# Performance work log

Measured on AMD Instinct MI355X. Metric: run time of the kernel, lower is better.

Reference implementation:

```python
import jax, jax.numpy as jnp
import numpy as np

PI = 3.14159  # literal used by the original module
N_QUBITS = 3
N_LAYERS = 2


def _apply_ry(state, theta, wire):
    """Apply RY(theta) on `wire`. state: (B, 2, 2, 2). theta: scalar or (B,)."""
    st = jnp.moveaxis(state, wire + 1, -1)
    c = jnp.cos(theta * 0.5)
    s = jnp.sin(theta * 0.5)
    nd = st.ndim - 1  # rank of st[..., 0]
    c = c.reshape(c.shape + (1,) * (nd - c.ndim))
    s = s.reshape(s.shape + (1,) * (nd - s.ndim))
    s0, s1 = st[..., 0], st[..., 1]
    st = jnp.stack([c * s0 - s * s1, s * s0 + c * s1], axis=-1)
    return jnp.moveaxis(st, -1, wire + 1)


def _apply_cnot(state, ctrl, tgt):
    """CNOT with control `ctrl`, target `tgt`: flip target where control=1."""
    st = jnp.moveaxis(state, (ctrl + 1, tgt + 1), (-2, -1))
    st = jnp.stack([st[..., 0, :], st[..., 1, ::-1]], axis=-2)
    return jnp.moveaxis(st, (-2, -1), (ctrl + 1, tgt + 1))


def _circuit(x, weights):
    B = x.shape[0]
    dt = x.dtype
    # |000...0> initial state, batched: (B, 2, 2, 2)
    state = jnp.zeros((B,) + (2,) * N_QUBITS, dt)
    state = state.at[(slice(None),) + (0,) * N_QUBITS].set(1.0)
    # angle encoding: RY(x[:, i] * pi) on wire i
    for i in range(N_QUBITS):
        state = _apply_ry(state, x[:, i] * PI, i)
    # variational layers: RY(weights[l, i]) then CNOT chain
    for l in range(N_LAYERS):
        for i in range(N_QUBITS):
            state = _apply_ry(state, weights[l, i], i)
        for i in range(N_QUBITS - 1):
            state = _apply_cnot(state, i, i + 1)
    # <Z_i> = sum_s |amp_s|^2 * (1 - 2*bit_i(s))  (RY/CNOT keep state real)
    probs = (state * state).reshape(B, 2 ** N_QUBITS)
    idx = jnp.arange(2 ** N_QUBITS)
    bits = (idx[None, :] >> (N_QUBITS - 1 - jnp.arange(N_QUBITS)[:, None])) & 1
    signs = (1.0 - 2.0 * bits).astype(dt)  # (n_qubits, 8)
    return probs @ signs.T  # (B, n_qubits)


def setup_inputs() -> dict:
    key = jax.random.key(0)
    k1, k2 = jax.random.split(key)
    x = jax.random.normal(k1, (2097152, 4), jnp.float32)
    weights = jax.random.normal(k2, (2, 3), jnp.float32) * 0.1
    return {"x": x, "weights": weights}


def reference(x, weights):
    return _circuit(x, weights)
```

## Files before the change

kernel.cpp:

```cpp
#include <hip/hip_runtime.h>


__global__ __launch_bounds__(256) void qfl_kernel(
    const float4* __restrict__ x, const float* __restrict__ w,
    float* __restrict__ out, int n)
{
    __shared__ float swc[6], sws[6];
    __shared__ float sout[768];
    const int tid = threadIdx.x;
    const long long b = (long long)blockIdx.x * 256 + tid;

    if (tid < 6) {
        float t = 0.5f * w[tid];
        sws[tid] = __sinf(t);
        swc[tid] = __cosf(t);
    }
    __syncthreads();

    float4 xv = (b < (long long)n) ? x[b] : make_float4(0.f, 0.f, 0.f, 0.f);

    const float HPI = 0.5f * 3.14159f;
    float a0, a1, b0, b1, c0, c1;
    __sincosf(xv.x * HPI, &a1, &a0);
    __sincosf(xv.y * HPI, &b1, &b0);
    __sincosf(xv.z * HPI, &c1, &c0);

    float st[8];
    st[0] = a0 * b0 * c0; st[1] = a0 * b0 * c1;
    st[2] = a0 * b1 * c0; st[3] = a0 * b1 * c1;
    st[4] = a1 * b0 * c0; st[5] = a1 * b0 * c1;
    st[6] = a1 * b1 * c0; st[7] = a1 * b1 * c1;

    #pragma unroll
    for (int l = 0; l < 2; ++l) {
        {
            float c = swc[l * 3 + 0], s = sws[l * 3 + 0];
            #pragma unroll
            for (int k = 0; k < 4; ++k) {
                float u = st[k], v = st[k + 4];
                st[k] = c * u - s * v; st[k + 4] = s * u + c * v;
            }
        }
        {
            float c = swc[l * 3 + 1], s = sws[l * 3 + 1];
            #pragma unroll
            for (int k = 0; k < 2; ++k) {
                float u = st[k],     v = st[k + 2];
                st[k]     = c * u  - s * v;  st[k + 2] = s * u  + c * v;
                float u2 = st[k + 4], v2 = st[k + 6];
                st[k + 4] = c * u2 - s * v2; st[k + 6] = s * u2 + c * v2;
            }
        }
        {
            float c = swc[l * 3 + 2], s = sws[l * 3 + 2];
            #pragma unroll
            for (int k = 0; k < 8; k += 2) {
                float u = st[k], v = st[k + 1];
                st[k] = c * u - s * v; st[k + 1] = s * u + c * v;
            }
        }
        { float t = st[4]; st[4] = st[6]; st[6] = t;
          t = st[5]; st[5] = st[7]; st[7] = t; }
        { float t = st[2]; st[2] = st[3]; st[3] = t;
          t = st[6]; st[6] = st[7]; st[7] = t; }
    }

    float p[8];
    #pragma unroll
    for (int k = 0; k < 8; ++k) p[k] = st[k] * st[k];
    float o0 = (p[0] + p[1] + p[2] + p[3]) - (p[4] + p[5] + p[6] + p[7]);
    float o1 = (p[0] + p[1] + p[4] + p[5]) - (p[2] + p[3] + p[6] + p[7]);
    float o2 = (p[0] + p[2] + p[4] + p[6]) - (p[1] + p[3] + p[5] + p[7]);

    sout[3 * tid + 0] = o0;
    sout[3 * tid + 1] = o1;
    sout[3 * tid + 2] = o2;
    __syncthreads();

    const long long base  = (long long)blockIdx.x * 768;
    const long long total = (long long)n * 3;
    #pragma unroll
    for (int k = 0; k < 3; ++k) {
        long long idx = base + k * 256 + tid;
        if (idx < total) out[idx] = sout[k * 256 + tid];
    }
}

extern "C" void kernel_launch(void* const* d_in, const int* in_sizes, int n_in,
                              void* d_out, int out_size, void* d_ws, size_t ws_size,
                              hipStream_t stream) {
    const float4* x = (const float4*)d_in[0];
    const float*  w = (const float*)d_in[1];
    float* out = (float*)d_out;
    int n = in_sizes[0] / 4;
    int blocks = (n + 255) / 256;
    qfl_kernel<<<blocks, 256, 0, stream>>>(x, w, out, n);
}
```

Measured before the change: 88.24 us.

## Fold first-layer RY into encoding angles, permute CNOTs symbolically, two elements per thread

The first variational RY layer is folded into the angle-encoding rotations by adding the half-weights to the encoding angles. The CNOT swaps are removed by relabeling the amplitudes, which leaves only three RY mixes on a product state. Each thread now processes two batch elements and writes float2 stores through shared memory, which halves the grid and removes the shared-memory weight precompute and its barrier. Every thread recomputes the sin/cos of the weights, which adds redundant transcendental work, and a separate odd-tail path handles the final element.

```diff
diff --git a/kernel.cpp b/kernel.cpp
--- a/kernel.cpp
+++ b/kernel.cpp
@@ -5,84 +5,75 @@
     const float4* __restrict__ x, const float* __restrict__ w,
     float* __restrict__ out, int n)
 {
-    __shared__ float swc[6], sws[6];
-    __shared__ float sout[768];
+    __shared__ float sout[1536];
     const int tid = threadIdx.x;
-    const long long b = (long long)blockIdx.x * 256 + tid;
+    const long long base = (long long)blockIdx.x * 512;
 
-    if (tid < 6) {
-        float t = 0.5f * w[tid];
-        sws[tid] = __sinf(t);
-        swc[tid] = __cosf(t);
+    const float hw0 = 0.5f * w[0], hw1 = 0.5f * w[1], hw2 = 0.5f * w[2];
+    const float c3 = __cosf(0.5f * w[3]), s3 = __sinf(0.5f * w[3]);
+    const float c4 = __cosf(0.5f * w[4]), s4 = __sinf(0.5f * w[4]);
+    const float c5 = __cosf(0.5f * w[5]), s5 = __sinf(0.5f * w[5]);
+
+    const float HPI = 0.5f * 3.14159f;
+
+    #pragma unroll
+    for (int half = 0; half < 2; ++half) {
+        const long long e = base + half * 256 + tid;
+        float4 xv = (e < (long long)n) ? x[e] : make_float4(0.f, 0.f, 0.f, 0.f);
+
+        float ta = fmaf(xv.x, HPI, hw0);
+        float tb = fmaf(xv.y, HPI, hw1);
+        float tc = fmaf(xv.z, HPI, hw2);
+        float a0 = __cosf(ta), a1 = __sinf(ta);
+        float b0 = __cosf(tb), b1 = __sinf(tb);
+        float c0 = __cosf(tc), c1 = __sinf(tc);
+
+        float a0b0 = a0 * b0, a0b1 = a0 * b1, a1b0 = a1 * b0, a1b1 = a1 * b1;
+        float v0 = a0b0 * c0, v1 = a0b0 * c1;
+        float v2 = a0b1 * c1, v3 = a0b1 * c0;
+        float v4 = a1b1 * c0, v5 = a1b1 * c1;
+        float v6 = a1b0 * c1, v7 = a1b0 * c0;
+
+        { float u, v;
+          u = v0; v = v4; v0 = c3*u - s3*v; v4 = s3*u + c3*v;
+          u = v1; v = v5; v1 = c3*u - s3*v; v5 = s3*u + c3*v;
+          u = v2; v = v6; v2 = c3*u - s3*v; v6 = s3*u + c3*v;
+          u = v3; v = v7; v3 = c3*u - s3*v; v7 = s3*u + c3*v; }
+        { float u, v;
+          u = v0; v = v2; v0 = c4*u - s4*v; v2 = s4*u + c4*v;
+          u = v1; v = v3; v1 = c4*u - s4*v; v3 = s4*u + c4*v;
+          u = v4; v = v6; v4 = c4*u - s4*v; v6 = s4*u + c4*v;
+          u = v5; v = v7; v5 = c4*u - s4*v; v7 = s4*u + c4*v; }
+        { float u, v;
+          u = v0; v = v1; v0 = c5*u - s5*v; v1 = s5*u + c5*v;
+          u = v2; v = v3; v2 = c5*u - s5*v; v3 = s5*u + c5*v;
+          u = v4; v = v5; v4 = c5*u - s5*v; v5 = s5*u + c5*v;
+          u = v6; v = v7; v6 = c5*u - s5*v; v7 = s5*u + c5*v; }
+
+        float q0 = v0*v0, q1 = v1*v1, q2 = v2*v2, q3 = v3*v3;
+        float q4 = v4*v4, q5 = v5*v5, q6 = v6*v6, q7 = v7*v7;
+        float o0 = (q0 + q1 + q2 + q3) - (q4 + q5 + q6 + q7);
+        float o1 = (q0 + q1 + q6 + q7) - (q2 + q3 + q4 + q5);
+        float o2 = (q0 + q3 + q5 + q6) - (q1 + q2 + q4 + q7);
+
+        sout[half * 768 + 3 * tid + 0] = o0;
+        sout[half * 768 + 3 * tid + 1] = o1;
+        sout[half * 768 + 3 * tid + 2] = o2;
     }
     __syncthreads();
 
-    float4 xv = (b < (long long)n) ? x[b] : make_float4(0.f, 0.f, 0.f, 0.f);
-
-    const float HPI = 0.5f * 3.14159f;
-    float a0, a1, b0, b1, c0, c1;
-    __sincosf(xv.x * HPI, &a1, &a0);
-    __sincosf(xv.y * HPI, &b1, &b0);
-    __sincosf(xv.z * HPI, &c1, &c0);
-
-    float st[8];
-    st[0] = a0 * b0 * c0; st[1] = a0 * b0 * c1;
-    st[2] = a0 * b1 * c0; st[3] = a0 * b1 * c1;
-    st[4] = a1 * b0 * c0; st[5] = a1 * b0 * c1;
-    st[6] = a1 * b1 * c0; st[7] = a1 * b1 * c1;
-
-    #pragma unroll
-    for (int l = 0; l < 2; ++l) {
-        {
-            float c = swc[l * 3 + 0], s = sws[l * 3 + 0];
-            #pragma unroll
-            for (int k = 0; k < 4; ++k) {
-                float u = st[k], v = st[k + 4];
-                st[k] = c * u - s * v; st[k + 4] = s * u + c * v;
-            }
-        }
-        {
-            float c = swc[l * 3 + 1], s = sws[l * 3 + 1];
-            #pragma unroll
-            for (int k = 0; k < 2; ++k) {
-                float u = st[k],     v = st[k + 2];
-                st[k]     = c * u  - s * v;  st[k + 2] = s * u  + c * v;
-                float u2 = st[k + 4], v2 = st[k + 6];
-                st[k + 4] = c * u2 - s * v2; st[k + 6] = s * u2 + c * v2;
-            }
-        }
-        {
-            float c = swc[l * 3 + 2], s = sws[l * 3 + 2];
-            #pragma unroll
-            for (int k = 0; k < 8; k += 2) {
-                float u = st[k], v = st[k + 1];
-                st[k] = c * u - s * v; st[k + 1] = s * u + c * v;
-            }
-        }
-        { float t = st[4]; st[4] = st[6]; st[6] = t;
-          t = st[5]; st[5] = st[7]; st[7] = t; }
-        { float t = st[2]; st[2] = st[3]; st[3] = t;
-          t = st[6]; st[6] = st[7]; st[7] = t; }
-    }
-
-    float p[8];
-    #pragma unroll
-    for (int k = 0; k < 8; ++k) p[k] = st[k] * st[k];
-    float o0 = (p[0] + p[1] + p[2] + p[3]) - (p[4] + p[5] + p[6] + p[7]);
-    float o1 = (p[0] + p[1] + p[4] + p[5]) - (p[2] + p[3] + p[6] + p[7]);
-    float o2 = (p[0] + p[2] + p[4] + p[6]) - (p[1] + p[3] + p[5] + p[7]);
-
-    sout[3 * tid + 0] = o0;
-    sout[3 * tid + 1] = o1;
-    sout[3 * tid + 2] = o2;
-    __syncthreads();
-
-    const long long base  = (long long)blockIdx.x * 768;
-    const long long total = (long long)n * 3;
+    const long long T  = (long long)n * 3;
+    const long long t2 = T >> 1;
+    const long long b2 = (long long)blockIdx.x * 768;
+    const float2* s2 = (const float2*)sout;
+    float2* og = (float2*)out;
     #pragma unroll
     for (int k = 0; k < 3; ++k) {
-        long long idx = base + k * 256 + tid;
-        if (idx < total) out[idx] = sout[k * 256 + tid];
+        long long idx = b2 + k * 256 + tid;
+        if (idx < t2) og[idx] = s2[k * 256 + tid];
+    }
+    if ((T & 1) && tid == 0 && blockIdx.x == gridDim.x - 1) {
+        out[T - 1] = sout[T - 1 - (long long)blockIdx.x * 1536];
     }
 }
 
@@ -93,6 +84,6 @@
     const float*  w = (const float*)d_in[1];
     float* out = (float*)d_out;
     int n = in_sizes[0] / 4;
-    int blocks = (n + 255) / 256;
+    int blocks = (n + 511) / 512;
     qfl_kernel<<<blocks, 256, 0, stream>>>(x, w, out, n);
 }
```

Result: faster. 81.80 us (-7.3%).
